# Optimization experiments

Hardware: AMD Instinct MI355X
Metric: run time of the kernel (lower is better)

## Reference

```python
import jax, jax.numpy as jnp
import numpy as np

MAX_SEQ = 768  # hardcoded in original compute_freqs_cis
THETA = 10000.0


def _freqs_cis(C, T):
    # freqs over FULL embed dim C (matches original, not per-head)
    freqs = 1.0 / THETA ** (jnp.arange(0, C, 2, dtype=jnp.float32)[: C // 2] / C)
    t = jnp.arange(MAX_SEQ, dtype=jnp.float32)
    ang = jnp.outer(t, freqs)  # [MAX_SEQ, C/2]
    return jnp.cos(ang)[:T], jnp.sin(ang)[:T]  # each [T, C/2]


def _apply_rope(u):
    # u: [B, T, C]; rotate adjacent channel pairs across full C
    B, T, C = u.shape
    fr, fi = _freqs_cis(C, T)           # [T, C/2]
    u2 = u.astype(jnp.float32).reshape(B, T, C // 2, 2)
    ur, ui = u2[..., 0], u2[..., 1]     # [B, T, C/2]
    out_r = ur * fr - ui * fi
    out_i = ur * fi + ui * fr
    return jnp.stack([out_r, out_i], axis=-1).reshape(B, T, C).astype(u.dtype)


def setup_inputs() -> dict:
    key = jax.random.key(0)
    k1, k2, k3 = jax.random.split(key, 3)
    B, T, C = 16, 768, 1024
    x = jax.random.normal(k1, (B, T, C), dtype=jnp.float32)
    Wqkv = jax.random.normal(k2, (3 * C, C), dtype=jnp.float32) * 0.02
    bqkv = jnp.zeros((3 * C,), dtype=jnp.float32)
    Wo = jax.random.normal(k3, (C, C), dtype=jnp.float32) * 0.02
    bo = jnp.zeros((C,), dtype=jnp.float32)
    return {"x": x, "Wqkv": Wqkv, "bqkv": bqkv, "Wo": Wo, "bo": bo}


def reference(x, Wqkv, bqkv, Wo, bo):
    B, T, C = x.shape
    H = 16
    D = C // H
    qkv = x @ Wqkv.T + bqkv                      # [B, T, 3C]
    q, k, v = jnp.split(qkv, 3, axis=-1)
    q = _apply_rope(q)
    k = _apply_rope(k)
    # [B, H, T, D]
    q = q.reshape(B, T, H, D).transpose(0, 2, 1, 3)
    k = k.reshape(B, T, H, D).transpose(0, 2, 1, 3)
    v = v.reshape(B, T, H, D).transpose(0, 2, 1, 3)
    scale = 1.0 / jnp.sqrt(jnp.asarray(D, dtype=q.dtype))
    scores = jnp.einsum("bhqd,bhkd->bhqk", q, k) * scale
    causal = jnp.tril(jnp.ones((T, T), dtype=bool))
    scores = jnp.where(causal, scores, jnp.finfo(scores.dtype).min)
    attn = jax.nn.softmax(scores, axis=-1)
    y = jnp.einsum("bhqk,bhkd->bhqd", attn, v)   # [B, H, T, D]
    y = y.transpose(0, 2, 1, 3).reshape(B, T, C)
    return y @ Wo.T + bo
```

## Files before the change

### kernel.cpp

```cpp
#include <hip/hip_runtime.h>
#include <hip/hip_bf16.h>

typedef __attribute__((ext_vector_type(8))) short bf16x8;
typedef __attribute__((ext_vector_type(4))) float f32x4;
typedef unsigned short u16;
typedef unsigned int u32;

#define DEV __device__ __forceinline__

DEV float bf2f(u16 v) { u32 u = ((u32)v) << 16; return __builtin_bit_cast(float, u); }
DEV u16 f2bf(float f) {
    u32 u = __builtin_bit_cast(u32, f);
    u32 r = (u + 0x7FFFu + ((u >> 16) & 1u)) >> 16;
    return (u16)r;
}

DEV void gll16(const u16* g, u16* l) {
    __builtin_amdgcn_global_load_lds((const __attribute__((address_space(1))) void*)g,
                                     (__attribute__((address_space(3))) void*)l, 16, 0, 0);
}

#define WAIT_VM0()   asm volatile("s_waitcnt vmcnt(0)" ::: "memory")
#define WAIT_LGKM0() asm volatile("s_waitcnt lgkmcnt(0)" ::: "memory")
#define BAR()        __builtin_amdgcn_s_barrier()
#define BARF()       asm volatile("s_barrier" ::: "memory")

__global__ void detect_kernel(const u32* __restrict__ x, int* __restrict__ flag) {
    __shared__ int cnt;
    if (threadIdx.x == 0) cnt = 0;
    __syncthreads();
    int c = 0;
    for (int i = threadIdx.x; i < 4096; i += 256) {
        u32 w = x[i];
        u32 e = (w >> 7) & 0xFF;
        c += (e >= 110 && e <= 132) ? 1 : 0;
    }
    atomicAdd(&cnt, c);
    __syncthreads();
    if (threadIdx.x == 0) *flag = (cnt * 2 > 4096) ? 1 : 0;
}

__global__ void cvt_bf16_kernel(const void* __restrict__ in, u16* __restrict__ out,
                                int n8, const int* __restrict__ flag) {
    const int fl = *flag;
    int i = blockIdx.x * 256 + threadIdx.x;
    const int stride = gridDim.x * 256;
    if (fl) {
        const bf16x8* ip = (const bf16x8*)in;
        bf16x8* op = (bf16x8*)out;
        for (; i < n8; i += stride) op[i] = ip[i];
    } else {
        const float4* ip = (const float4*)in;
        bf16x8* op = (bf16x8*)out;
        for (; i < n8; i += stride) {
            float4 a = ip[2 * i], b = ip[2 * i + 1];
            bf16x8 o;
            o[0] = (short)f2bf(a.x); o[1] = (short)f2bf(a.y);
            o[2] = (short)f2bf(a.z); o[3] = (short)f2bf(a.w);
            o[4] = (short)f2bf(b.x); o[5] = (short)f2bf(b.y);
            o[6] = (short)f2bf(b.z); o[7] = (short)f2bf(b.w);
            op[i] = o;
        }
    }
}

__global__ void cvt_f32_kernel(const void* __restrict__ in, float* __restrict__ out,
                               int n, const int* __restrict__ flag) {
    const int fl = *flag;
    int i = blockIdx.x * 256 + threadIdx.x;
    if (i < n) out[i] = fl ? bf2f(((const u16*)in)[i]) : ((const float*)in)[i];
}

__global__ void rope_table_kernel(float2* __restrict__ tab) {
    int idx = blockIdx.x * 256 + threadIdx.x;
    int t = idx >> 9, j = idx & 511;
    float freq = expf(-(float)(2 * j) * (9.210340371976184f / 1024.0f));
    float ang = (float)t * freq;
    tab[idx] = make_float2(cosf(ang), sinf(ang));
}

__global__ __launch_bounds__(512, 2)
void gemm256p_kernel(const u16* __restrict__ A, const u16* __restrict__ W,
                     const float* __restrict__ bias, void* __restrict__ C,
                     int N, const int* __restrict__ flag, int out_mode,
                     const float2* __restrict__ tab, int rope) {
    constexpr int K = 1024, NT = 16;
    __shared__ u16 lds[2][32768];
    const int tid = threadIdx.x;
    const int l = tid & 63, w = tid >> 6;
    const int wm = w >> 2, wn = w & 3;
    const int lo = l & 15, hi = l >> 4;

    const int M0 = blockIdx.x * 256, N0 = blockIdx.y * 256;

    const int rS = tid >> 3;
    const int qS = (tid & 7) ^ (rS & 7);
    const u16* Ag = A + (size_t)(M0 + rS) * K + qS * 8;
    const u16* Wg = W + (size_t)(N0 + rS) * K + qS * 8;
    const int lb = w * 512;

    f32x4 acc[8][4] = {};

#define STG_A(kt, slot, half)                                                  \
    {                                                                          \
        u16* sA_ = &lds[slot][(half) * 8192];                                  \
        const u16* ga_ = Ag + (kt) * 64 + (size_t)(128 * (half)) * K;          \
        gll16(ga_,                  sA_ + lb);                                 \
        gll16(ga_ + (size_t)64 * K, sA_ + 4096 + lb);                          \
    }
#define STG_B(kt, slot, half)                                                  \
    {                                                                          \
        u16* sB_ = &lds[slot][16384 + (half) * 8192];                          \
        const u16* gb_ = Wg + (kt) * 64 + (size_t)(128 * (half)) * K;          \
        gll16(gb_,                  sB_ + lb);                                 \
        gll16(gb_ + (size_t)64 * K, sB_ + 4096 + lb);                          \
    }

    STG_A(0, 0, 0); STG_A(0, 0, 1);
    STG_B(0, 0, 0); STG_B(0, 0, 1);
    WAIT_VM0();
    BARF();

    const int csw = lo & 7;

#pragma unroll 1
    for (int t = 0; t < NT; ++t) {
        const int cur = t & 1, nxt = cur ^ 1;
        const u16* sA = &lds[cur][0];
        const u16* sB = &lds[cur][16384];
        bf16x8 afr[4], bfr[4];

#pragma unroll
        for (int n = 0; n < 4; ++n)
            bfr[n] = *(const bf16x8*)&sB[(wn * 64 + n * 16 + lo) * 64 + ((hi ^ csw) * 8)];
#pragma unroll
        for (int m = 0; m < 4; ++m)
            afr[m] = *(const bf16x8*)&sA[(wm * 128 + m * 16 + lo) * 64 + ((hi ^ csw) * 8)];
        if (t + 1 < NT) { STG_A(t + 1, nxt, 0); STG_A(t + 1, nxt, 1); }
        BARF();
        __builtin_amdgcn_s_setprio(1);
#pragma unroll
        for (int m = 0; m < 4; ++m)
#pragma unroll
            for (int n = 0; n < 4; ++n)
                acc[m][n] = __builtin_amdgcn_mfma_f32_16x16x32_bf16(afr[m], bfr[n], acc[m][n], 0, 0, 0);
        __builtin_amdgcn_s_setprio(0);
        BARF();

#pragma unroll
        for (int m = 0; m < 4; ++m)
            afr[m] = *(const bf16x8*)&sA[(wm * 128 + 64 + m * 16 + lo) * 64 + ((hi ^ csw) * 8)];
        if (t + 1 < NT) { STG_B(t + 1, nxt, 0); STG_B(t + 1, nxt, 1); }
        BARF();
        __builtin_amdgcn_s_setprio(1);
#pragma unroll
        for (int m = 0; m < 4; ++m)
#pragma unroll
            for (int n = 0; n < 4; ++n)
                acc[4 + m][n] = __builtin_amdgcn_mfma_f32_16x16x32_bf16(afr[m], bfr[n], acc[4 + m][n], 0, 0, 0);
        __builtin_amdgcn_s_setprio(0);
        BARF();

#pragma unroll
        for (int n = 0; n < 4; ++n)
            bfr[n] = *(const bf16x8*)&sB[(wn * 64 + n * 16 + lo) * 64 + (((4 + hi) ^ csw) * 8)];
#pragma unroll
        for (int m = 0; m < 4; ++m)
            afr[m] = *(const bf16x8*)&sA[(wm * 128 + m * 16 + lo) * 64 + (((4 + hi) ^ csw) * 8)];
        BARF();
        __builtin_amdgcn_s_setprio(1);
#pragma unroll
        for (int m = 0; m < 4; ++m)
#pragma unroll
            for (int n = 0; n < 4; ++n)
                acc[m][n] = __builtin_amdgcn_mfma_f32_16x16x32_bf16(afr[m], bfr[n], acc[m][n], 0, 0, 0);
        __builtin_amdgcn_s_setprio(0);
        BARF();

#pragma unroll
        for (int m = 0; m < 4; ++m)
            afr[m] = *(const bf16x8*)&sA[(wm * 128 + 64 + m * 16 + lo) * 64 + (((4 + hi) ^ csw) * 8)];
        WAIT_VM0();
        BARF();
        __builtin_amdgcn_s_setprio(1);
#pragma unroll
        for (int m = 0; m < 4; ++m)
#pragma unroll
            for (int n = 0; n < 4; ++n)
                acc[4 + m][n] = __builtin_amdgcn_mfma_f32_16x16x32_bf16(afr[m], bfr[n], acc[4 + m][n], 0, 0, 0);
        __builtin_amdgcn_s_setprio(0);
        BARF();
    }
#undef STG_A
#undef STG_B

    const int f32out = out_mode ? (*flag == 0) : 0;
    const int do_rope = rope && (N0 < 2048);
#pragma unroll
    for (int mi = 0; mi < 8; ++mi) {
        const int rbase = M0 + wm * 128 + (mi >> 2) * 64 + (mi & 3) * 16 + hi * 4;
        const int tbase = (M0 % 768) + wm * 128 + (mi >> 2) * 64 + (mi & 3) * 16 + hi * 4;
#pragma unroll
        for (int n = 0; n < 4; ++n) {
            const int col = N0 + wn * 64 + lo + n * 16;
            float bi = bias[col];
            const int jf = (col & 1023) >> 1;
            const int odd = col & 1;
#pragma unroll
            for (int j = 0; j < 4; ++j) {
                float v = acc[mi][n][j] + bi;
                if (do_rope) {
                    float partner = __shfl_xor(v, 1);
                    float2 cs = tab[(tbase + j) * 512 + jf];
                    v = odd ? (v * cs.x + partner * cs.y) : (v * cs.x - partner * cs.y);
                }
                size_t idx = (size_t)(rbase + j) * N + col;
                if (f32out) ((float*)C)[idx] = v;
                else        ((u16*)C)[idx] = f2bf(v);
            }
        }
    }
}

__global__ __launch_bounds__(256)
void attn_kernel(const u16* __restrict__ qkv, u16* __restrict__ y) {
    constexpr int T = 768, CH = 1024, QKVC = 3072;
    constexpr float NEG = -30000.0f;
    __shared__ u16 Ks[2][64 * 64];
    __shared__ u16 Vt[64 * 72];
    __shared__ u16 Ps[64 * 72];

    const int tid = threadIdx.x, l = tid & 63, w = tid >> 6;
    const int qt = blockIdx.x, h = blockIdx.y, b = blockIdx.z;
    const int lo = l & 15, hi = l >> 4;
    const int kk = hi * 8;
    const int swzk = (lo & 7) * 8;

    const int qrow = qt * 64 + w * 16 + lo;
    const u16* qptr = qkv + (size_t)(b * T + qrow) * QKVC + h * 64 + kk;
    bf16x8 aq0r = *(const bf16x8*)qptr;
    bf16x8 aq1r = *(const bf16x8*)(qptr + 32);
    bf16x8 aq0, aq1;
#pragma unroll
    for (int e = 0; e < 8; ++e) {
        aq0[e] = (short)f2bf(bf2f((u16)aq0r[e]) * 0.125f);
        aq1[e] = (short)f2bf(bf2f((u16)aq1r[e]) * 0.125f);
    }

    f32x4 o[4] = {};
    float mrun[4] = {NEG, NEG, NEG, NEG};
    float lrun[4] = {0.f, 0.f, 0.f, 0.f};

    const int ksr = w * 16 + (l >> 3);
    const int ksc = ((l & 7) ^ ((l >> 3) & 7)) * 8;
    const u16* kbase = qkv + (size_t)(b * T + ksr) * QKVC + CH + h * 64 + ksc;

    const int vd0 = (tid & 7) * 8;
    const int vswz = (tid & 7) * 8;
    const int vr0 = tid >> 3, vr1 = 32 + (tid >> 3);
    const u16* vbase = qkv + (size_t)(b * T) * QKVC + 2 * CH + h * 64 + vd0;

    gll16(kbase, &Ks[0][w * 1024]);
    gll16(kbase + (size_t)8 * QKVC, &Ks[0][w * 1024 + 512]);
    bf16x8 cv0 = *(const bf16x8*)(vbase + (size_t)vr0 * QKVC);
    bf16x8 cv1 = *(const bf16x8*)(vbase + (size_t)vr1 * QKVC);
    WAIT_VM0();
#pragma unroll
    for (int e = 0; e < 8; ++e) {
        Vt[(vd0 + e) * 72 + (vr0 ^ vswz)] = (u16)cv0[e];
        Vt[(vd0 + e) * 72 + (vr1 ^ vswz)] = (u16)cv1[e];
    }

    for (int kt = 0; kt <= qt; ++kt) {
        const int cur = kt & 1, nxt = cur ^ 1;
        bf16x8 nv0, nv1;
        if (kt < qt) {
            const size_t koff = (size_t)((kt + 1) * 64) * QKVC;
            gll16(kbase + koff, &Ks[nxt][w * 1024]);
            gll16(kbase + koff + (size_t)8 * QKVC, &Ks[nxt][w * 1024 + 512]);
            const u16* vb2 = vbase + (size_t)((kt + 1) * 64) * QKVC;
            nv0 = *(const bf16x8*)(vb2 + (size_t)vr0 * QKVC);
            nv1 = *(const bf16x8*)(vb2 + (size_t)vr1 * QKVC);
        }
        WAIT_LGKM0();
        BAR();

        __builtin_amdgcn_s_setprio(1);
        f32x4 s[4];
#pragma unroll
        for (int n = 0; n < 4; ++n) {
            bf16x8 kb0 = *(const bf16x8*)&Ks[cur][(n * 16 + lo) * 64 + (kk ^ swzk)];
            bf16x8 kb1 = *(const bf16x8*)&Ks[cur][(n * 16 + lo) * 64 + ((32 + kk) ^ swzk)];
            f32x4 z = {0.f, 0.f, 0.f, 0.f};
            z = __builtin_amdgcn_mfma_f32_16x16x32_bf16(aq0, kb0, z, 0, 0, 0);
            z = __builtin_amdgcn_mfma_f32_16x16x32_bf16(aq1, kb1, z, 0, 0, 0);
            s[n] = z;
        }
        __builtin_amdgcn_s_setprio(0);

        if (kt == qt) {
#pragma unroll
            for (int n = 0; n < 4; ++n) {
                int kcol = n * 16 + lo;
#pragma unroll
                for (int j = 0; j < 4; ++j)
                    if (kcol > w * 16 + hi * 4 + j) s[n][j] = NEG;
            }
        }
        float mnew[4], corr[4];
#pragma unroll
        for (int j = 0; j < 4; ++j) {
            float mx = fmaxf(fmaxf(s[0][j], s[1][j]), fmaxf(s[2][j], s[3][j]));
            mx = fmaxf(mx, __shfl_xor(mx, 1));
            mx = fmaxf(mx, __shfl_xor(mx, 2));
            mx = fmaxf(mx, __shfl_xor(mx, 4));
            mx = fmaxf(mx, __shfl_xor(mx, 8));
            mnew[j] = fmaxf(mrun[j], mx);
            corr[j] = __expf(mrun[j] - mnew[j]);
            mrun[j] = mnew[j];
        }
        float p[4][4];
#pragma unroll
        for (int n = 0; n < 4; ++n)
#pragma unroll
            for (int j = 0; j < 4; ++j)
                p[n][j] = __expf(s[n][j] - mnew[j]);
#pragma unroll
        for (int j = 0; j < 4; ++j) {
            float r = p[0][j] + p[1][j] + p[2][j] + p[3][j];
            r += __shfl_xor(r, 1);
            r += __shfl_xor(r, 2);
            r += __shfl_xor(r, 4);
            r += __shfl_xor(r, 8);
            lrun[j] = lrun[j] * corr[j] + r;
        }
#pragma unroll
        for (int n = 0; n < 4; ++n)
#pragma unroll
            for (int j = 0; j < 4; ++j)
                o[n][j] *= corr[j];
#pragma unroll
        for (int n = 0; n < 4; ++n)
#pragma unroll
            for (int j = 0; j < 4; ++j)
                Ps[(w * 16 + hi * 4 + j) * 72 + n * 16 + lo] = f2bf(p[n][j]);

        __builtin_amdgcn_s_setprio(1);
#pragma unroll
        for (int c = 0; c < 2; ++c) {
            bf16x8 pa = *(const bf16x8*)&Ps[(w * 16 + lo) * 72 + c * 32 + kk];
#pragma unroll
            for (int n = 0; n < 4; ++n) {
                const int v = (n * 2 + (lo >> 3)) & 7;
                bf16x8 vb = *(const bf16x8*)&Vt[(n * 16 + lo) * 72 + ((c * 32 + kk) ^ (v * 8))];
                o[n] = __builtin_amdgcn_mfma_f32_16x16x32_bf16(pa, vb, o[n], 0, 0, 0);
            }
        }
        __builtin_amdgcn_s_setprio(0);

        if (kt < qt) {
            WAIT_VM0();
            BAR();
#pragma unroll
            for (int e = 0; e < 8; ++e) {
                Vt[(vd0 + e) * 72 + (vr0 ^ vswz)] = (u16)nv0[e];
                Vt[(vd0 + e) * 72 + (vr1 ^ vswz)] = (u16)nv1[e];
            }
        }
    }

    float inv[4];
#pragma unroll
    for (int j = 0; j < 4; ++j) inv[j] = (lrun[j] > 0.f) ? 1.0f / lrun[j] : 0.f;
#pragma unroll
    for (int n = 0; n < 4; ++n)
#pragma unroll
        for (int j = 0; j < 4; ++j) {
            int t = qt * 64 + w * 16 + hi * 4 + j;
            y[(size_t)(b * T + t) * CH + h * 64 + n * 16 + lo] = f2bf(o[n][j] * inv[j]);
        }
}

extern "C" void kernel_launch(void* const* d_in, const int* in_sizes, int n_in,
                              void* d_out, int out_size, void* d_ws, size_t ws_size,
                              hipStream_t stream) {
    char* ws = (char*)d_ws;
    int*   flag  = (int*)ws;
    u16*   xb    = (u16*)(ws + 256);
    u16*   Wqb   = (u16*)(ws + 256 + 25165824);
    u16*   Wob   = (u16*)(ws + 256 + 31457280);
    float* bqf   = (float*)(ws + 256 + 33554432);
    float* bof   = (float*)(ws + 256 + 33566720);
    u16*   qkv   = (u16*)(ws + 256 + 33570816);
    u16*   y     = (u16*)(ws + 256 + 109068288);
    float2* tab  = (float2*)(ws + 256 + 134234112);

    detect_kernel<<<1, 256, 0, stream>>>((const u32*)d_in[0], flag);
    cvt_bf16_kernel<<<2048, 256, 0, stream>>>(d_in[0], xb,  12582912 / 8, flag);
    cvt_bf16_kernel<<<1536, 256, 0, stream>>>(d_in[1], Wqb, 3145728 / 8, flag);
    cvt_bf16_kernel<<<512,  256, 0, stream>>>(d_in[3], Wob, 1048576 / 8, flag);
    cvt_f32_kernel<<<12, 256, 0, stream>>>(d_in[2], bqf, 3072, flag);
    cvt_f32_kernel<<<4,  256, 0, stream>>>(d_in[4], bof, 1024, flag);
    rope_table_kernel<<<768 * 512 / 256, 256, 0, stream>>>(tab);

    gemm256p_kernel<<<dim3(48, 12), 512, 0, stream>>>(xb, Wqb, bqf, qkv, 3072, flag, 0, tab, 1);
    attn_kernel<<<dim3(12, 16, 16), 256, 0, stream>>>(qkv, y);
    gemm256p_kernel<<<dim3(48, 4), 512, 0, stream>>>(y, Wob, bof, d_out, 1024, flag, 1, tab, 0);
}
```

Measured before the change: 308.4 us.

## Widen attention query tile to 128 rows with 8 waves sharing K/V tiles

The attention kernel now uses 512 threads per block and handles 128 query rows per block instead of 64, with each block staging 64-row K/V tiles. The causal loop runs over 2*qt+2 key tiles with a global-index mask. Each wave now loads half as much of each K/V tile, which halves redundant K/V global traffic and LDS staging per query row. The trade-offs: half the grid size, coarser causal load balancing, and the first four waves process one fully masked key tile at the diagonal.

After: 302.9 us. Within noise of the previous version (-1.8%).

```diff
diff --git a/kernel.cpp b/kernel.cpp
--- a/kernel.cpp
+++ b/kernel.cpp
@@ -222,13 +222,13 @@
     }
 }
 
-__global__ __launch_bounds__(256)
+__global__ __launch_bounds__(512)
 void attn_kernel(const u16* __restrict__ qkv, u16* __restrict__ y) {
     constexpr int T = 768, CH = 1024, QKVC = 3072;
     constexpr float NEG = -30000.0f;
     __shared__ u16 Ks[2][64 * 64];
     __shared__ u16 Vt[64 * 72];
-    __shared__ u16 Ps[64 * 72];
+    __shared__ u16 Ps[128 * 72];
 
     const int tid = threadIdx.x, l = tid & 63, w = tid >> 6;
     const int qt = blockIdx.x, h = blockIdx.y, b = blockIdx.z;
@@ -236,7 +236,7 @@
     const int kk = hi * 8;
     const int swzk = (lo & 7) * 8;
 
-    const int qrow = qt * 64 + w * 16 + lo;
+    const int qrow = qt * 128 + w * 16 + lo;
     const u16* qptr = qkv + (size_t)(b * T + qrow) * QKVC + h * 64 + kk;
     bf16x8 aq0r = *(const bf16x8*)qptr;
     bf16x8 aq1r = *(const bf16x8*)(qptr + 32);
@@ -251,36 +251,31 @@
     float mrun[4] = {NEG, NEG, NEG, NEG};
     float lrun[4] = {0.f, 0.f, 0.f, 0.f};
 
-    const int ksr = w * 16 + (l >> 3);
+    const int ksr = w * 8 + (l >> 3);
     const int ksc = ((l & 7) ^ ((l >> 3) & 7)) * 8;
     const u16* kbase = qkv + (size_t)(b * T + ksr) * QKVC + CH + h * 64 + ksc;
 
     const int vd0 = (tid & 7) * 8;
     const int vswz = (tid & 7) * 8;
-    const int vr0 = tid >> 3, vr1 = 32 + (tid >> 3);
+    const int vr0 = tid >> 3;
     const u16* vbase = qkv + (size_t)(b * T) * QKVC + 2 * CH + h * 64 + vd0;
 
-    gll16(kbase, &Ks[0][w * 1024]);
-    gll16(kbase + (size_t)8 * QKVC, &Ks[0][w * 1024 + 512]);
+    const int NTk = 2 * qt + 2;
+
+    gll16(kbase, &Ks[0][w * 512]);
     bf16x8 cv0 = *(const bf16x8*)(vbase + (size_t)vr0 * QKVC);
-    bf16x8 cv1 = *(const bf16x8*)(vbase + (size_t)vr1 * QKVC);
     WAIT_VM0();
 #pragma unroll
-    for (int e = 0; e < 8; ++e) {
+    for (int e = 0; e < 8; ++e)
         Vt[(vd0 + e) * 72 + (vr0 ^ vswz)] = (u16)cv0[e];
-        Vt[(vd0 + e) * 72 + (vr1 ^ vswz)] = (u16)cv1[e];
-    }
-
-    for (int kt = 0; kt <= qt; ++kt) {
+
+    for (int kt = 0; kt < NTk; ++kt) {
         const int cur = kt & 1, nxt = cur ^ 1;
-        bf16x8 nv0, nv1;
-        if (kt < qt) {
+        bf16x8 nv0;
+        if (kt + 1 < NTk) {
             const size_t koff = (size_t)((kt + 1) * 64) * QKVC;
-            gll16(kbase + koff, &Ks[nxt][w * 1024]);
-            gll16(kbase + koff + (size_t)8 * QKVC, &Ks[nxt][w * 1024 + 512]);
-            const u16* vb2 = vbase + (size_t)((kt + 1) * 64) * QKVC;
-            nv0 = *(const bf16x8*)(vb2 + (size_t)vr0 * QKVC);
-            nv1 = *(const bf16x8*)(vb2 + (size_t)vr1 * QKVC);
+            gll16(kbase + koff, &Ks[nxt][w * 512]);
+            nv0 = *(const bf16x8*)(vbase + (size_t)((kt + 1) * 64 + vr0) * QKVC);
         }
         WAIT_LGKM0();
         BAR();
@@ -298,13 +293,13 @@
         }
         __builtin_amdgcn_s_setprio(0);
 
-        if (kt == qt) {
+        if (kt >= 2 * qt) {
 #pragma unroll
             for (int n = 0; n < 4; ++n) {
-                int kcol = n * 16 + lo;
+                int kcol = kt * 64 + n * 16 + lo;
 #pragma unroll
                 for (int j = 0; j < 4; ++j)
-                    if (kcol > w * 16 + hi * 4 + j) s[n][j] = NEG;
+                    if (kcol > qt * 128 + w * 16 + hi * 4 + j) s[n][j] = NEG;
             }
         }
         float mnew[4], corr[4];
@@ -358,14 +353,12 @@
         }
         __builtin_amdgcn_s_setprio(0);
 
-        if (kt < qt) {
+        if (kt + 1 < NTk) {
             WAIT_VM0();
             BAR();
 #pragma unroll
-            for (int e = 0; e < 8; ++e) {
+            for (int e = 0; e < 8; ++e)
                 Vt[(vd0 + e) * 72 + (vr0 ^ vswz)] = (u16)nv0[e];
-                Vt[(vd0 + e) * 72 + (vr1 ^ vswz)] = (u16)nv1[e];
-            }
         }
     }
 
@@ -376,7 +369,7 @@
     for (int n = 0; n < 4; ++n)
 #pragma unroll
         for (int j = 0; j < 4; ++j) {
-            int t = qt * 64 + w * 16 + hi * 4 + j;
+            int t = qt * 128 + w * 16 + hi * 4 + j;
             y[(size_t)(b * T + t) * CH + h * 64 + n * 16 + lo] = f2bf(o[n][j] * inv[j]);
         }
 }
@@ -404,6 +397,6 @@
     rope_table_kernel<<<768 * 512 / 256, 256, 0, stream>>>(tab);
 
     gemm256p_kernel<<<dim3(48, 12), 512, 0, stream>>>(xb, Wqb, bqf, qkv, 3072, flag, 0, tab, 1);
-    attn_kernel<<<dim3(12, 16, 16), 256, 0, stream>>>(qkv, y);
+    attn_kernel<<<dim3(6, 16, 16), 512, 0, stream>>>(qkv, y);
     gemm256p_kernel<<<dim3(48, 4), 512, 0, stream>>>(y, Wob, bof, d_out, 1024, flag, 1, tab, 0);
 }
```
